# Kernel tuning notes

Measured on AMD Instinct MI355X. Metric: run time of the kernel, lower is better.

## Reference

```python
import jax, jax.numpy as jnp
import numpy as np

NUM_EMBED = 512
EMBED_DIM = 64
COMMITMENT_COST = 0.25
DECAY = 0.99
LAPLACE_ALPHA = 1e-05


def setup_inputs() -> dict:
    key = jax.random.key(0)
    k1, k2 = jax.random.split(key, 2)
    inputs = jax.random.normal(k1, (4, EMBED_DIM, 32, 32, 32), dtype=jnp.float32)
    embed = jax.random.normal(k2, (NUM_EMBED, EMBED_DIM), dtype=jnp.float32)
    # buffers: embed_avg starts as a clone of embed; cluster_size at steady state (post first pass)
    embed_avg = embed
    cluster_size = jnp.ones((NUM_EMBED,), dtype=jnp.float32)
    return {"inputs": inputs, "embed": embed, "embed_avg": embed_avg, "cluster_size": cluster_size}


def reference(inputs, embed, embed_avg, cluster_size):
    # channel-last flatten: [B,C,D,H,W] -> [B,D,H,W,C] -> [N,C]
    channel_last = jnp.transpose(inputs, (0, 2, 3, 4, 1))
    input_shape = channel_last.shape
    flat_input = channel_last.reshape(-1, EMBED_DIM)  # [N, C]
    n_tokens = flat_input.shape[0]

    distances = ((flat_input ** 2).sum(axis=1, keepdims=True)
                 + (embed ** 2).sum(axis=1)
                 - 2.0 * flat_input @ embed.T)
    encoding_indices = jnp.argmin(distances, axis=1)  # [N]

    quantized_cl = embed[encoding_indices].reshape(input_shape)  # gather + reshape

    # --- EMA codebook update (training branch), all non-differentiable ---
    # new_cluster_size = one_hot.sum(0); dw = one_hot.T @ flat_input  (as segment sums)
    new_counts = jax.ops.segment_sum(jnp.ones((n_tokens,), flat_input.dtype),
                                     encoding_indices, num_segments=NUM_EMBED)
    dw = jax.ops.segment_sum(flat_input, encoding_indices, num_segments=NUM_EMBED)  # [K, C]
    new_cluster_size = cluster_size * DECAY + (1.0 - DECAY) * new_counts
    new_embed_avg = embed_avg * DECAY + (1.0 - DECAY) * dw
    n = new_cluster_size.sum()
    smoothed = n * ((new_cluster_size + LAPLACE_ALPHA) / (n + NUM_EMBED * LAPLACE_ALPHA))
    new_embed = new_embed_avg / smoothed[:, None]

    # perplexity from empirical code usage
    avg_probs = new_counts / n_tokens
    perplexity = jnp.exp(-jnp.sum(avg_probs * jnp.log(avg_probs + 1e-10)))

    quantized_cf = jnp.transpose(quantized_cl, (0, 4, 1, 2, 3))  # back to [B,C,D,H,W]

    # commitment loss (quantized is detached in original; everything above is no_grad)
    e_latent_loss = jnp.mean((quantized_cf - inputs) ** 2)
    loss = COMMITMENT_COST * e_latent_loss

    # straight-through estimator
    quantized_out = inputs + jax.lax.stop_gradient(quantized_cf - inputs)

    encoding_indices = encoding_indices.reshape(input_shape[:-1])
    return (loss, quantized_out, perplexity, encoding_indices,
            new_embed, new_cluster_size, new_embed_avg)
```

## Files before the change

### kernel.cpp

```cpp
#include <hip/hip_runtime.h>
#include <math.h>

typedef __attribute__((ext_vector_type(8))) short s16x8;
typedef __attribute__((ext_vector_type(4))) float f32x4;

#define B_    4
#define C_    64
#define S_    32768
#define N_    131072
#define K_    512
#define SPLITS 8
#define DECAY_ 0.99f
#define ONEM_  0.01f
#define ALPHA_ 1e-5f
#define DELTA_ 0.01f
#define AMB_CAP 65536

#define OFF_LOSS 0
#define OFF_Q    1
#define OFF_PERP 8388609
#define OFF_IDX  8388610
#define OFF_NEMB 8519682
#define OFF_NCS  8552450
#define OFF_NEA  8552962

#define WS_LOSS   0
#define WS_AMBN   8
#define WS_CNT    16
#define WS_CUR    528
#define WS_OFFS   1040
#define WS_SMOOTH 1552
#define WS_E2     2064
#define WS_SORT   2576
#define WS_PART   133648
#define WS_SPL    395792
#define WS_AMB    444944
#define WS_ET     510480

__device__ __forceinline__ ushort f2bf(float f) {
    uint u = __float_as_uint(f);
    u = u + 0x7FFFu + ((u >> 16) & 1u);
    return (ushort)(u >> 16);
}
__device__ __forceinline__ float bf2f(ushort h) {
    return __uint_as_float(((uint)h) << 16);
}

__global__ __launch_bounds__(256) void k_split(const float* __restrict__ embed,
                                               float* __restrict__ wsf,
                                               int* __restrict__ wsi) {
    const int t = threadIdx.x;
    const int lane = t & 63;
    const int code = blockIdx.x * 4 + (t >> 6);
    if (blockIdx.x == 0) {
        for (int i = t; i < WS_OFFS; i += 256) wsi[i] = 0;
    }
    const float e = embed[code * C_ + lane];
    const float sc = -2.f * e;
    const ushort h1 = f2bf(sc);
    const ushort h2 = f2bf(sc - bf2f(h1));
    ushort* tab = (ushort*)(wsf + WS_SPL);
    tab[0 * (K_ * C_) + code * C_ + lane] = h1;
    tab[1 * (K_ * C_) + code * C_ + lane] = h2;
    wsf[WS_ET + lane * K_ + code] = e;
    float sq = e * e;
    for (int o = 32; o > 0; o >>= 1) sq += __shfl_down(sq, o, 64);
    if (lane == 0) wsf[WS_E2 + code] = sq;
}

__global__ __launch_bounds__(256) void k_assign(const float* __restrict__ in,
                                                float* __restrict__ out,
                                                float* __restrict__ wsf,
                                                int* __restrict__ wsi) {
    __shared__ float s_e2l[K_];
    __shared__ int   s_cnt[K_];
    __shared__ float s_x2[256];
    __shared__ float s_loss;

    const int t = threadIdx.x;
    const int lane = t & 63;
    const int w = t >> 6;
    const int col = lane & 15;
    const int quad = lane >> 4;

    for (int i = t; i < K_; i += 256) { s_e2l[i] = wsf[WS_E2 + i]; s_cnt[i] = 0; }
    if (t == 0) s_loss = 0.f;

    const int nw = blockIdx.x * 256 + w * 64;

    s16x8 a[4][2][2];
#pragma unroll
    for (int j = 0; j < 4; ++j) {
        const int n = nw + j * 16 + col;
        const int base = ((n >> 15) << 21) + (n & (S_ - 1));
        float x0[8], x1[8];
#pragma unroll
        for (int q = 0; q < 8; ++q) {
            x0[q] = in[base + ((quad * 8 + q) << 15)];
            x1[q] = in[base + ((32 + quad * 8 + q) << 15)];
        }
        float x2 = 0.f;
#pragma unroll
        for (int q = 0; q < 8; ++q) x2 += x0[q] * x0[q] + x1[q] * x1[q];
        x2 += __shfl_xor(x2, 16, 64);
        x2 += __shfl_xor(x2, 32, 64);
        if (quad == 0) s_x2[w * 64 + j * 16 + col] = x2;

        float4* q0 = (float4*)(out + OFF_Q + (size_t)n * C_ + quad * 8);
        q0[0] = make_float4(x0[0], x0[1], x0[2], x0[3]);
        q0[1] = make_float4(x0[4], x0[5], x0[6], x0[7]);
        float4* q1 = (float4*)(out + OFF_Q + (size_t)n * C_ + 32 + quad * 8);
        q1[0] = make_float4(x1[0], x1[1], x1[2], x1[3]);
        q1[1] = make_float4(x1[4], x1[5], x1[6], x1[7]);

#pragma unroll
        for (int q = 0; q < 8; ++q) {
            ushort h = f2bf(x0[q]); a[j][0][0][q] = (short)h;
            a[j][1][0][q] = (short)f2bf(x0[q] - bf2f(h));
            h = f2bf(x1[q]); a[j][0][1][q] = (short)h;
            a[j][1][1][q] = (short)f2bf(x1[q] - bf2f(h));
        }
    }
    __syncthreads();

    const s16x8* tab = (const s16x8*)(wsf + WS_SPL);
    float bestd[4][4], bestd2[4][4];
    int   besti[4][4];
#pragma unroll
    for (int j = 0; j < 4; ++j)
#pragma unroll
        for (int r = 0; r < 4; ++r) { bestd[j][r] = 3.4e38f; bestd2[j][r] = 3.4e38f; besti[j][r] = 0; }

    int o = col * 8 + quad;
    s16x8 bh0 = tab[o], bh1 = tab[o + 4];
    s16x8 bl0 = tab[4096 + o], bl1 = tab[4096 + o + 4];

    for (int ct = 0; ct < 32; ++ct) {
        s16x8 nh0, nh1, nl0, nl1;
        if (ct < 31) {
            const int on = o + 128;
            nh0 = tab[on];        nh1 = tab[on + 4];
            nl0 = tab[4096 + on]; nl1 = tab[4096 + on + 4];
        }
        const float e2c = s_e2l[ct * 16 + col];
        f32x4 acc[4];
#pragma unroll
        for (int j = 0; j < 4; ++j) acc[j] = (f32x4){e2c, e2c, e2c, e2c};
#pragma unroll
        for (int j = 0; j < 4; ++j) acc[j] = __builtin_amdgcn_mfma_f32_16x16x32_bf16(a[j][1][0], bh0, acc[j], 0, 0, 0);
#pragma unroll
        for (int j = 0; j < 4; ++j) acc[j] = __builtin_amdgcn_mfma_f32_16x16x32_bf16(a[j][1][1], bh1, acc[j], 0, 0, 0);
#pragma unroll
        for (int j = 0; j < 4; ++j) acc[j] = __builtin_amdgcn_mfma_f32_16x16x32_bf16(a[j][0][0], bl0, acc[j], 0, 0, 0);
#pragma unroll
        for (int j = 0; j < 4; ++j) acc[j] = __builtin_amdgcn_mfma_f32_16x16x32_bf16(a[j][0][1], bl1, acc[j], 0, 0, 0);
#pragma unroll
        for (int j = 0; j < 4; ++j) acc[j] = __builtin_amdgcn_mfma_f32_16x16x32_bf16(a[j][0][0], bh0, acc[j], 0, 0, 0);
#pragma unroll
        for (int j = 0; j < 4; ++j) acc[j] = __builtin_amdgcn_mfma_f32_16x16x32_bf16(a[j][0][1], bh1, acc[j], 0, 0, 0);

        const int code = ct * 16 + col;
#pragma unroll
        for (int j = 0; j < 4; ++j) {
#pragma unroll
            for (int r = 0; r < 4; ++r) {
                const float av = acc[j][r];
                bestd2[j][r] = fminf(bestd2[j][r], fmaxf(av, bestd[j][r]));
                if (av < bestd[j][r]) { bestd[j][r] = av; besti[j][r] = code; }
            }
        }
        bh0 = nh0; bh1 = nh1; bl0 = nl0; bl1 = nl1;
        o += 128;
    }

    float lsum = 0.f;
#pragma unroll
    for (int j = 0; j < 4; ++j) {
#pragma unroll
        for (int r = 0; r < 4; ++r) {
            float d1 = bestd[j][r], d2 = bestd2[j][r]; int i1 = besti[j][r];
            for (int m = 1; m <= 8; m <<= 1) {
                const float d1o = __shfl_xor(d1, m, 64);
                const int   i1o = __shfl_xor(i1, m, 64);
                const float d2o = __shfl_xor(d2, m, 64);
                if (d1o < d1 || (d1o == d1 && i1o < i1)) {
                    d2 = fminf(d1, d2o); d1 = d1o; i1 = i1o;
                } else {
                    d2 = fminf(d2, d1o);
                }
            }
            if (col == 0) {
                const int tok = j * 16 + quad * 4 + r;
                out[OFF_IDX + nw + tok] = (float)i1;
                atomicAdd(&s_cnt[i1], 1);
                lsum += d1 + s_x2[w * 64 + tok];
                if (d2 - d1 < DELTA_) {
                    const int pos = atomicAdd(&wsi[WS_AMBN], 1);
                    if (pos < AMB_CAP) wsi[WS_AMB + pos] = nw + tok;
                }
            }
        }
    }
    if (col == 0) atomicAdd(&s_loss, lsum);
    __syncthreads();
    for (int i = t; i < K_; i += 256) {
        const int v = s_cnt[i];
        if (v) atomicAdd(&wsi[WS_CNT + i], v);
    }
    if (t == 0) atomicAdd(&wsf[WS_LOSS], s_loss);
}

__global__ __launch_bounds__(256) void k_fixup(float* __restrict__ out,
                                               const float* __restrict__ wsf,
                                               int* __restrict__ wsi) {
    __shared__ float sx[4][C_];
    const int t = threadIdx.x;
    const int lane = t & 63;
    const int w = t >> 6;
    const int gw = blockIdx.x * 4 + w;
    const int nw = gridDim.x * 4;
    int cntA = wsi[WS_AMBN];
    if (cntA > AMB_CAP) cntA = AMB_CAP;
    const float* eT = wsf + WS_ET;

    for (int a = gw; a < cntA; a += nw) {
        const int n = wsi[WS_AMB + a];
        const float xv = out[OFF_Q + (size_t)n * C_ + lane];
        sx[w][lane] = xv;
        float x2 = xv * xv;
        for (int m = 1; m <= 32; m <<= 1) x2 += __shfl_xor(x2, m, 64);

        float bd = 3.4e38f; int bi = 0;
#pragma unroll 2
        for (int q = 0; q < 8; ++q) {
            const int k = (q << 6) + lane;
            float d0 = 0.f, d1 = 0.f, d2 = 0.f, d3 = 0.f;
#pragma unroll
            for (int c = 0; c < C_; c += 4) {
                d0 += sx[w][c + 0] * eT[(c + 0) * K_ + k];
                d1 += sx[w][c + 1] * eT[(c + 1) * K_ + k];
                d2 += sx[w][c + 2] * eT[(c + 2) * K_ + k];
                d3 += sx[w][c + 3] * eT[(c + 3) * K_ + k];
            }
            const float dist = x2 + wsf[WS_E2 + k] - 2.f * ((d0 + d1) + (d2 + d3));
            if (dist < bd) { bd = dist; bi = k; }
        }
        for (int m = 1; m <= 32; m <<= 1) {
            const float db = __shfl_xor(bd, m, 64);
            const int   ib = __shfl_xor(bi, m, 64);
            if (db < bd || (db == bd && ib < bi)) { bd = db; bi = ib; }
        }
        if (lane == 0) {
            const int old = (int)out[OFF_IDX + n];
            if (bi != old) {
                out[OFF_IDX + n] = (float)bi;
                atomicAdd(&wsi[WS_CNT + old], -1);
                atomicAdd(&wsi[WS_CNT + bi], 1);
            }
        }
    }
}

#define SCT 256
__global__ __launch_bounds__(256) void k_scatter(const float* __restrict__ out,
                                                 int* __restrict__ wsi) {
    __shared__ int sA[K_];
    __shared__ int sB[K_];
    __shared__ int lc[K_];
    const int t = threadIdx.x;
    const int base = blockIdx.x * SCT;

    const int c0 = wsi[WS_CNT + t];
    const int c1 = wsi[WS_CNT + t + 256];
    sA[t] = c0; sA[t + 256] = c1;
    __syncthreads();
    int* sa = sA; int* sb = sB;
    for (int o = 1; o < K_; o <<= 1) {
        const int va = sa[t]       + ((t >= o)       ? sa[t - o]       : 0);
        const int vb = sa[t + 256] + ((t + 256 >= o) ? sa[t + 256 - o] : 0);
        sb[t] = va; sb[t + 256] = vb;
        __syncthreads();
        int* tmp = sa; sa = sb; sb = tmp;
    }
    const int offs0 = sa[t] - c0;
    const int offs1 = sa[t + 256] - c1;
    if (blockIdx.x == 0) { wsi[WS_OFFS + t] = offs0; wsi[WS_OFFS + t + 256] = offs1; }

    int* hist = sb;
    hist[t] = 0; hist[t + 256] = 0;
    lc[t] = 0;  lc[t + 256] = 0;
    __syncthreads();
    const int kc = (int)out[OFF_IDX + base + t];
    atomicAdd(&hist[kc], 1);
    __syncthreads();
    const int ha = hist[t];
    const int hb = hist[t + 256];
    int ga = 0, gb = 0;
    if (ha > 0) ga = atomicAdd(&wsi[WS_CUR + t], ha);
    if (hb > 0) gb = atomicAdd(&wsi[WS_CUR + t + 256], hb);
    __syncthreads();
    hist[t] = offs0 + ga;
    hist[t + 256] = offs1 + gb;
    __syncthreads();
    const int pos = atomicAdd(&lc[kc], 1);
    wsi[WS_SORT + hist[kc] + pos] = base + t;
}

__global__ __launch_bounds__(64) void k_dw_split(float* __restrict__ out,
                                                 float* __restrict__ wsf,
                                                 const int* __restrict__ wsi) {
    const int lane = threadIdx.x;
    const int k = blockIdx.x >> 3;
    const int p = blockIdx.x & (SPLITS - 1);
    const int off = wsi[WS_OFFS + k];
    const int cnt = wsi[WS_CNT + k];
    const int chunk = (cnt + SPLITS - 1) >> 3;
    const int j0 = p * chunk;
    const int j1 = min(j0 + chunk, cnt);
    const float* fx = out + OFF_Q;
    const int* sort = wsi + WS_SORT + off;

    float acc = 0.f;
    for (int base = j0; base < j1; base += 64) {
        const int mcnt = min(64, j1 - base);
        int id = 0;
        if (base + lane < j1) id = sort[base + lane];
        int m = 0;
        for (; m + 8 <= mcnt; m += 8) {
            const int t0 = __shfl(id, m + 0, 64);
            const int t1 = __shfl(id, m + 1, 64);
            const int t2 = __shfl(id, m + 2, 64);
            const int t3 = __shfl(id, m + 3, 64);
            const int t4 = __shfl(id, m + 4, 64);
            const int t5 = __shfl(id, m + 5, 64);
            const int t6 = __shfl(id, m + 6, 64);
            const int t7 = __shfl(id, m + 7, 64);
            const float v0 = fx[(size_t)t0 * C_ + lane];
            const float v1 = fx[(size_t)t1 * C_ + lane];
            const float v2 = fx[(size_t)t2 * C_ + lane];
            const float v3 = fx[(size_t)t3 * C_ + lane];
            const float v4 = fx[(size_t)t4 * C_ + lane];
            const float v5 = fx[(size_t)t5 * C_ + lane];
            const float v6 = fx[(size_t)t6 * C_ + lane];
            const float v7 = fx[(size_t)t7 * C_ + lane];
            acc += ((v0 + v1) + (v2 + v3)) + ((v4 + v5) + (v6 + v7));
        }
        for (; m < mcnt; ++m) {
            const int tk = __shfl(id, m, 64);
            acc += fx[(size_t)tk * C_ + lane];
        }
    }
    wsf[WS_PART + (size_t)blockIdx.x * C_ + lane] = acc;
}

__global__ __launch_bounds__(256) void k_emaq(const float* __restrict__ embed,
                                              const float* __restrict__ embed_avg,
                                              const float* __restrict__ cs,
                                              float* __restrict__ out,
                                              const float* __restrict__ wsf,
                                              const int* __restrict__ wsi) {
    __shared__ float sn[256];
    __shared__ float sncs[K_];
    const int t = threadIdx.x;
    const int bid = blockIdx.x;

    const int c0 = wsi[WS_CNT + t];
    const int c1 = wsi[WS_CNT + t + 256];
    const float ncs0 = cs[t] * DECAY_ + ONEM_ * (float)c0;
    const float ncs1 = cs[t + 256] * DECAY_ + ONEM_ * (float)c1;
    sncs[t] = ncs0; sncs[t + 256] = ncs1;
    sn[t] = ncs0 + ncs1;
    __syncthreads();
    for (int o = 128; o > 0; o >>= 1) { if (t < o) sn[t] += sn[t + o]; __syncthreads(); }
    const float ntot = sn[0];
    __syncthreads();

    if (bid == 0) {
        out[OFF_NCS + t] = ncs0;
        out[OFF_NCS + t + 256] = ncs1;
        const float ap0 = (float)c0 / (float)N_;
        const float ap1 = (float)c1 / (float)N_;
        sn[t] = ap0 * logf(ap0 + 1e-10f) + ap1 * logf(ap1 + 1e-10f);
        __syncthreads();
        for (int o = 128; o > 0; o >>= 1) { if (t < o) sn[t] += sn[t + o]; __syncthreads(); }
        if (t == 0) {
            out[OFF_PERP] = expf(-sn[0]);
            out[OFF_LOSS] = 0.25f * wsf[WS_LOSS] / (float)((long long)N_ * C_);
        }
    }

    if (bid < 128) {
        const int i = bid * 256 + t;
        const int k = i >> 6;
        const int c = i & 63;
        const float smooth = ntot * (sncs[k] + ALPHA_) / (ntot + (float)K_ * ALPHA_);
        float dw = 0.f;
#pragma unroll
        for (int p = 0; p < SPLITS; ++p)
            dw += wsf[WS_PART + (size_t)(k * SPLITS + p) * C_ + c];
        const float nea = embed_avg[i] * DECAY_ + ONEM_ * dw;
        out[OFF_NEA + i] = nea;
        out[OFF_NEMB + i] = nea / smooth;
    }

    const int n = bid * 256 + t;
    const int b = n >> 15;
    const int s = n & (S_ - 1);
    const int qbase = (b << 21) + s;
    const int k = (int)out[OFF_IDX + n];
    const float4* er = (const float4*)(embed + k * C_);
#pragma unroll
    for (int q = 0; q < 16; ++q) {
        float4 v = er[q];
        out[OFF_Q + qbase + ((4 * q + 0) << 15)] = v.x;
        out[OFF_Q + qbase + ((4 * q + 1) << 15)] = v.y;
        out[OFF_Q + qbase + ((4 * q + 2) << 15)] = v.z;
        out[OFF_Q + qbase + ((4 * q + 3) << 15)] = v.w;
    }
}

extern "C" void kernel_launch(void* const* d_in, const int* in_sizes, int n_in,
                              void* d_out, int out_size, void* d_ws, size_t ws_size,
                              hipStream_t stream) {
    const float* in        = (const float*)d_in[0];
    const float* embed     = (const float*)d_in[1];
    const float* embed_avg = (const float*)d_in[2];
    const float* cs        = (const float*)d_in[3];
    float* out = (float*)d_out;
    float* wsf = (float*)d_ws;
    int*   wsi = (int*)d_ws;

    k_split   <<<K_ / 4, 256, 0, stream>>>(embed, wsf, wsi);
    k_assign  <<<N_ / 256, 256, 0, stream>>>(in, out, wsf, wsi);
    k_fixup   <<<256, 256, 0, stream>>>(out, wsf, wsi);
    k_scatter <<<N_ / SCT, 256, 0, stream>>>(out, wsi);
    k_dw_split<<<K_ * SPLITS, 64, 0, stream>>>(out, wsf, wsi);
    k_emaq    <<<N_ / 256, 256, 0, stream>>>(embed, embed_avg, cs, out, wsf, wsi);
}
```

Before: 208.0 us.

## Replace sort-based segment sum with float atomics into replicated accumulators

```diff
diff --git a/kernel.cpp b/kernel.cpp
--- a/kernel.cpp
+++ b/kernel.cpp
@@ -9,7 +9,7 @@
 #define S_    32768
 #define N_    131072
 #define K_    512
-#define SPLITS 8
+#define DWP   4
 #define DECAY_ 0.99f
 #define ONEM_  0.01f
 #define ALPHA_ 1e-5f
@@ -29,7 +29,6 @@
 #define WS_CNT    16
 #define WS_CUR    528
 #define WS_OFFS   1040
-#define WS_SMOOTH 1552
 #define WS_E2     2064
 #define WS_SORT   2576
 #define WS_PART   133648
@@ -55,6 +54,9 @@
     if (blockIdx.x == 0) {
         for (int i = t; i < WS_OFFS; i += 256) wsi[i] = 0;
     }
+    for (int i = blockIdx.x * 256 + t; i < DWP * K_ * C_; i += 128 * 256)
+        wsf[WS_PART + i] = 0.f;
+
     const float e = embed[code * C_ + lane];
     const float sc = -2.f * e;
     const ushort h1 = f2bf(sc);
@@ -261,96 +263,23 @@
     }
 }
 
-#define SCT 256
-__global__ __launch_bounds__(256) void k_scatter(const float* __restrict__ out,
-                                                 int* __restrict__ wsi) {
-    __shared__ int sA[K_];
-    __shared__ int sB[K_];
-    __shared__ int lc[K_];
-    const int t = threadIdx.x;
-    const int base = blockIdx.x * SCT;
-
-    const int c0 = wsi[WS_CNT + t];
-    const int c1 = wsi[WS_CNT + t + 256];
-    sA[t] = c0; sA[t + 256] = c1;
-    __syncthreads();
-    int* sa = sA; int* sb = sB;
-    for (int o = 1; o < K_; o <<= 1) {
-        const int va = sa[t]       + ((t >= o)       ? sa[t - o]       : 0);
-        const int vb = sa[t + 256] + ((t + 256 >= o) ? sa[t + 256 - o] : 0);
-        sb[t] = va; sb[t + 256] = vb;
-        __syncthreads();
-        int* tmp = sa; sa = sb; sb = tmp;
-    }
-    const int offs0 = sa[t] - c0;
-    const int offs1 = sa[t + 256] - c1;
-    if (blockIdx.x == 0) { wsi[WS_OFFS + t] = offs0; wsi[WS_OFFS + t + 256] = offs1; }
-
-    int* hist = sb;
-    hist[t] = 0; hist[t + 256] = 0;
-    lc[t] = 0;  lc[t + 256] = 0;
-    __syncthreads();
-    const int kc = (int)out[OFF_IDX + base + t];
-    atomicAdd(&hist[kc], 1);
-    __syncthreads();
-    const int ha = hist[t];
-    const int hb = hist[t + 256];
-    int ga = 0, gb = 0;
-    if (ha > 0) ga = atomicAdd(&wsi[WS_CUR + t], ha);
-    if (hb > 0) gb = atomicAdd(&wsi[WS_CUR + t + 256], hb);
-    __syncthreads();
-    hist[t] = offs0 + ga;
-    hist[t + 256] = offs1 + gb;
-    __syncthreads();
-    const int pos = atomicAdd(&lc[kc], 1);
-    wsi[WS_SORT + hist[kc] + pos] = base + t;
-}
-
-__global__ __launch_bounds__(64) void k_dw_split(float* __restrict__ out,
-                                                 float* __restrict__ wsf,
-                                                 const int* __restrict__ wsi) {
-    const int lane = threadIdx.x;
-    const int k = blockIdx.x >> 3;
-    const int p = blockIdx.x & (SPLITS - 1);
-    const int off = wsi[WS_OFFS + k];
-    const int cnt = wsi[WS_CNT + k];
-    const int chunk = (cnt + SPLITS - 1) >> 3;
-    const int j0 = p * chunk;
-    const int j1 = min(j0 + chunk, cnt);
+__global__ __launch_bounds__(256) void k_dw_atomic(const float* __restrict__ out,
+                                                   float* __restrict__ wsf) {
+    const int t = threadIdx.x;
+    const int lane = t & 63;
+    const int w = t >> 6;
+    const int gw = blockIdx.x * 4 + w;
+    const int tok0 = gw * 64;
     const float* fx = out + OFF_Q;
-    const int* sort = wsi + WS_SORT + off;
-
-    float acc = 0.f;
-    for (int base = j0; base < j1; base += 64) {
-        const int mcnt = min(64, j1 - base);
-        int id = 0;
-        if (base + lane < j1) id = sort[base + lane];
-        int m = 0;
-        for (; m + 8 <= mcnt; m += 8) {
-            const int t0 = __shfl(id, m + 0, 64);
-            const int t1 = __shfl(id, m + 1, 64);
-            const int t2 = __shfl(id, m + 2, 64);
-            const int t3 = __shfl(id, m + 3, 64);
-            const int t4 = __shfl(id, m + 4, 64);
-            const int t5 = __shfl(id, m + 5, 64);
-            const int t6 = __shfl(id, m + 6, 64);
-            const int t7 = __shfl(id, m + 7, 64);
-            const float v0 = fx[(size_t)t0 * C_ + lane];
-            const float v1 = fx[(size_t)t1 * C_ + lane];
-            const float v2 = fx[(size_t)t2 * C_ + lane];
-            const float v3 = fx[(size_t)t3 * C_ + lane];
-            const float v4 = fx[(size_t)t4 * C_ + lane];
-            const float v5 = fx[(size_t)t5 * C_ + lane];
-            const float v6 = fx[(size_t)t6 * C_ + lane];
-            const float v7 = fx[(size_t)t7 * C_ + lane];
-            acc += ((v0 + v1) + (v2 + v3)) + ((v4 + v5) + (v6 + v7));
-        }
-        for (; m < mcnt; ++m) {
-            const int tk = __shfl(id, m, 64);
-            acc += fx[(size_t)tk * C_ + lane];
-        }
-    }
-    wsf[WS_PART + (size_t)blockIdx.x * C_ + lane] = acc;
+    float* acc = wsf + WS_PART + (size_t)(blockIdx.x & (DWP - 1)) * (K_ * C_);
+
+    const int myidx = (int)out[OFF_IDX + tok0 + lane];
+#pragma unroll 4
+    for (int m = 0; m < 64; ++m) {
+        const int k = __shfl(myidx, m, 64);
+        const float v = fx[(size_t)(tok0 + m) * C_ + lane];
+        atomicAdd(&acc[k * C_ + lane], v);
+    }
 }
 
 __global__ __launch_bounds__(256) void k_emaq(const float* __restrict__ embed,
@@ -392,12 +321,11 @@
     if (bid < 128) {
         const int i = bid * 256 + t;
         const int k = i >> 6;
-        const int c = i & 63;
         const float smooth = ntot * (sncs[k] + ALPHA_) / (ntot + (float)K_ * ALPHA_);
         float dw = 0.f;
 #pragma unroll
-        for (int p = 0; p < SPLITS; ++p)
-            dw += wsf[WS_PART + (size_t)(k * SPLITS + p) * C_ + c];
+        for (int p = 0; p < DWP; ++p)
+            dw += wsf[WS_PART + (size_t)p * (K_ * C_) + i];
         const float nea = embed_avg[i] * DECAY_ + ONEM_ * dw;
         out[OFF_NEA + i] = nea;
         out[OFF_NEMB + i] = nea / smooth;
@@ -430,10 +358,9 @@
     float* wsf = (float*)d_ws;
     int*   wsi = (int*)d_ws;
 
-    k_split   <<<K_ / 4, 256, 0, stream>>>(embed, wsf, wsi);
-    k_assign  <<<N_ / 256, 256, 0, stream>>>(in, out, wsf, wsi);
-    k_fixup   <<<256, 256, 0, stream>>>(out, wsf, wsi);
-    k_scatter <<<N_ / SCT, 256, 0, stream>>>(out, wsi);
-    k_dw_split<<<K_ * SPLITS, 64, 0, stream>>>(out, wsf, wsi);
-    k_emaq    <<<N_ / 256, 256, 0, stream>>>(embed, embed_avg, cs, out, wsf, wsi);
-}
+    k_split    <<<K_ / 4, 256, 0, stream>>>(embed, wsf, wsi);
+    k_assign   <<<N_ / 256, 256, 0, stream>>>(in, out, wsf, wsi);
+    k_fixup    <<<256, 256, 0, stream>>>(out, wsf, wsi);
+    k_dw_atomic<<<N_ / 256, 256, 0, stream>>>(out, wsf);
+    k_emaq     <<<N_ / 256, 256, 0, stream>>>(embed, embed_avg, cs, out, wsf, wsi);
+}
```

Result: slower. 223.8 us (+7.6%).
